# Kernel tuning notes

Hardware: AMD Instinct MI355X
Metric: run time of the kernel (lower is better)

Reference implementation:

```python
import jax, jax.numpy as jnp
import numpy as np

INPUT_DIM = 100
LATENT_DIM = 128
HIDDEN_DIM = 64
BATCH = 16384


def setup_inputs() -> dict:
    key = jax.random.key(0)
    ku, k1, kb1, k2, kb2 = jax.random.split(key, 5)
    u = jax.random.normal(ku, (BATCH, INPUT_DIM), dtype=jnp.float32)
    # PyTorch Linear init: U(-1/sqrt(fan_in), 1/sqrt(fan_in))
    s1 = 1.0 / np.sqrt(INPUT_DIM)
    s2 = 1.0 / np.sqrt(HIDDEN_DIM)
    W1 = jax.random.uniform(k1, (LATENT_DIM, HIDDEN_DIM, INPUT_DIM), jnp.float32, -s1, s1)
    b1 = jax.random.uniform(kb1, (LATENT_DIM, HIDDEN_DIM), jnp.float32, -s1, s1)
    W2 = jax.random.uniform(k2, (LATENT_DIM, HIDDEN_DIM), jnp.float32, -s2, s2)  # out_features=1 squeezed
    b2 = jax.random.uniform(kb2, (LATENT_DIM,), jnp.float32, -s2, s2)
    return {"u": u, "W1": W1, "b1": b1, "W2": W2, "b2": b2}


def reference(u, W1, b1, W2, b2):
    # All latent_dim branches batched as one grouped GEMM.
    # h: [batch, latent, hidden]
    h = jnp.tanh(jnp.einsum('bi,khi->bkh', u, W1) + b1[None, :, :])
    # out: [batch, latent]  (second Linear has output dim 1, squeezed)
    out = jnp.einsum('bkh,kh->bk', h, W2) + b2[None, :]
    return out
```

## Files before the change

### kernel.cpp

```cpp
#include <hip/hip_runtime.h>

#define BATCH 16384
#define LATENT 128
#define HIDDEN 64
#define INDIM 100
#define KPAD 128
#define TANH_SCALE 2.885390081777927f

typedef short shortx8 __attribute__((ext_vector_type(8)));
typedef float floatx4 __attribute__((ext_vector_type(4)));

__device__ __forceinline__ short f2bf(float f) {
    union { float f; unsigned u; } v; v.f = f;
    unsigned r = v.u + 0x7FFF + ((v.u >> 16) & 1);
    return (short)(r >> 16);
}

#if __has_builtin(__builtin_amdgcn_exp2f)
#define EXP2F(x) __builtin_amdgcn_exp2f(x)
#else
#define EXP2F(x) __exp2f(x)
#endif
#if __has_builtin(__builtin_amdgcn_rcpf)
#define RCPF(x) __builtin_amdgcn_rcpf(x)
#else
#define RCPF(x) (1.0f / (x))
#endif

#define N_U_CHUNKS (BATCH * KPAD / 8)
#define N_W_CHUNKS (LATENT * HIDDEN * KPAD / 8)

__global__ __launch_bounds__(256) void prep_all(const float* __restrict__ u,
                                                const float* __restrict__ W1,
                                                const float* __restrict__ b1,
                                                const float* __restrict__ W2,
                                                const float* __restrict__ b2,
                                                shortx8* __restrict__ uf,
                                                shortx8* __restrict__ wf,
                                                float* __restrict__ b2eff) {
    int c = blockIdx.x * 256 + threadIdx.x;
    if (c < N_U_CHUNKS) {
        int lane = c & 63;
        int kt = (c >> 6) & 3;
        int g = c >> 8;
        int row = g * 16 + (lane & 15);
        int kbase = kt * 32 + ((lane >> 4) << 3);
        shortx8 v;
        if (kbase + 7 < INDIM) {
            const float4* p = (const float4*)(u + row * INDIM + kbase);
            float4 f0 = p[0], f1 = p[1];
            v[0] = f2bf(f0.x); v[1] = f2bf(f0.y); v[2] = f2bf(f0.z); v[3] = f2bf(f0.w);
            v[4] = f2bf(f1.x); v[5] = f2bf(f1.y); v[6] = f2bf(f1.z); v[7] = f2bf(f1.w);
        } else {
#pragma unroll
            for (int j = 0; j < 8; j++) {
                int k = kbase + j;
                float f = (k < INDIM) ? u[row * INDIM + k] : (k == INDIM ? 1.0f : 0.0f);
                v[j] = f2bf(f);
            }
        }
        uf[c] = v;
    } else if (c < N_U_CHUNKS + N_W_CHUNKS) {
        int c2 = c - N_U_CHUNKS;
        int lane = c2 & 63;
        int kt = (c2 >> 6) & 3;
        int nt = (c2 >> 8) & 3;
        int lat = c2 >> 10;
        int h = nt * 16 + (lane & 15);
        int hw = lat * HIDDEN + h;
        int kbase = kt * 32 + ((lane >> 4) << 3);
        shortx8 v;
        if (kbase + 7 < INDIM) {
            const float4* p = (const float4*)(W1 + hw * INDIM + kbase);
            float4 f0 = p[0], f1 = p[1];
            v[0] = f2bf(f0.x * TANH_SCALE); v[1] = f2bf(f0.y * TANH_SCALE);
            v[2] = f2bf(f0.z * TANH_SCALE); v[3] = f2bf(f0.w * TANH_SCALE);
            v[4] = f2bf(f1.x * TANH_SCALE); v[5] = f2bf(f1.y * TANH_SCALE);
            v[6] = f2bf(f1.z * TANH_SCALE); v[7] = f2bf(f1.w * TANH_SCALE);
        } else {
#pragma unroll
            for (int j = 0; j < 8; j++) {
                int k = kbase + j;
                float f = (k < INDIM) ? W1[hw * INDIM + k] * TANH_SCALE
                                      : (k == INDIM ? b1[hw] * TANH_SCALE : 0.0f);
                v[j] = f2bf(f);
            }
        }
        wf[c2] = v;
    } else {
        int lat = c - (N_U_CHUNKS + N_W_CHUNKS);
        if (lat < LATENT) {
            float s = b2[lat];
            const float* wp = W2 + lat * HIDDEN;
#pragma unroll 8
            for (int h = 0; h < HIDDEN; h++) s += wp[h];
            b2eff[lat] = s;
        }
    }
}

__global__ __launch_bounds__(256, 4) void branch_mlp(const shortx8* __restrict__ uf,
                                                     const shortx8* __restrict__ wf,
                                                     const float* __restrict__ W2,
                                                     const float* __restrict__ b2eff,
                                                     float* __restrict__ out) {
    int tid = threadIdx.x;
    int lane = tid & 63;
    int w = tid >> 6;
    int bx = blockIdx.x;
    int lat = bx >> 5;
    int G0 = (bx & 31) * 32 + w * 8;
    int q = lane >> 4;

    shortx8 afr[4][4];
    const shortx8* wb = wf + (size_t)lat * 16 * 64 + lane;
#pragma unroll
    for (int nt = 0; nt < 4; nt++)
#pragma unroll
        for (int kt = 0; kt < 4; kt++)
            afr[nt][kt] = wb[(nt * 4 + kt) * 64];

    float4 w2v[4];
#pragma unroll
    for (int nt = 0; nt < 4; nt++) {
        float4 t = *(const float4*)(W2 + lat * HIDDEN + nt * 16 + q * 4);
        w2v[nt] = make_float4(-2.0f * t.x, -2.0f * t.y, -2.0f * t.z, -2.0f * t.w);
    }
    float b2v = b2eff[lat];

    const shortx8* ua = uf + (size_t)G0 * 4 * 64 + lane;
    float* outp = out + (size_t)G0 * 16 * LATENT + lat;

#pragma unroll
    for (int g = 0; g < 8; g++) {
        shortx8 ub[4];
#pragma unroll
        for (int kt = 0; kt < 4; kt++)
            ub[kt] = ua[(g * 4 + kt) * 64];

        floatx4 acc[4] = {};
#pragma unroll
        for (int kt = 0; kt < 4; kt++)
#pragma unroll
            for (int nt = 0; nt < 4; nt++)
                acc[nt] = __builtin_amdgcn_mfma_f32_16x16x32_bf16(afr[nt][kt], ub[kt], acc[nt], 0, 0, 0);

        float s = 0.0f;
#pragma unroll
        for (int nt = 0; nt < 4; nt++)
#pragma unroll
            for (int r = 0; r < 4; r++) {
                float e = EXP2F(acc[nt][r]);
                float rr = RCPF(e + 1.0f);
                s = fmaf((&w2v[nt].x)[r], rr, s);
            }
        s += __shfl_xor(s, 16, 64);
        s += __shfl_xor(s, 32, 64);
        if (lane < 16)
            outp[(g * 16 + lane) * LATENT] = s + b2v;
    }
}

__global__ __launch_bounds__(256) void fallback_kernel(const float* __restrict__ u, const float* __restrict__ W1,
                                                       const float* __restrict__ b1, const float* __restrict__ W2,
                                                       const float* __restrict__ b2, float* __restrict__ out) {
    int idx = blockIdx.x * 256 + threadIdx.x;
    if (idx >= BATCH * LATENT) return;
    int b = idx >> 7;
    int lat = idx & 127;
    const float* ub = u + b * INDIM;
    float s = 0.0f;
    for (int h = 0; h < HIDDEN; h++) {
        const float* wp = W1 + (lat * HIDDEN + h) * INDIM;
        float dd = b1[lat * HIDDEN + h];
        for (int k = 0; k < INDIM; k++) dd += ub[k] * wp[k];
        s += tanhf(dd) * W2[lat * HIDDEN + h];
    }
    out[idx] = s + b2[lat];
}

extern "C" void kernel_launch(void* const* d_in, const int* in_sizes, int n_in,
                              void* d_out, int out_size, void* d_ws, size_t ws_size,
                              hipStream_t stream) {
    const float* u  = (const float*)d_in[0];
    const float* W1 = (const float*)d_in[1];
    const float* b1 = (const float*)d_in[2];
    const float* W2 = (const float*)d_in[3];
    const float* b2 = (const float*)d_in[4];
    float* out = (float*)d_out;

    const size_t UF_BYTES = (size_t)BATCH * KPAD * 2;
    const size_t WF_BYTES = (size_t)LATENT * HIDDEN * KPAD * 2;
    const size_t B2_BYTES = LATENT * sizeof(float);

    if (ws_size < UF_BYTES + WF_BYTES + B2_BYTES) {
        fallback_kernel<<<(BATCH * LATENT + 255) / 256, 256, 0, stream>>>(u, W1, b1, W2, b2, out);
        return;
    }

    shortx8* uf = (shortx8*)d_ws;
    shortx8* wf = (shortx8*)((char*)d_ws + UF_BYTES);
    float* b2eff = (float*)((char*)d_ws + UF_BYTES + WF_BYTES);

    prep_all<<<(N_U_CHUNKS + N_W_CHUNKS) / 256 + 1, 256, 0, stream>>>(u, W1, b1, W2, b2, uf, wf, b2eff);
    branch_mlp<<<4096, 256, 0, stream>>>(uf, wf, W2, b2eff, out);
}
```

Baseline: 111.7 us.

## Split hidden dimension across waves and reduce partial sums in shared memory

```diff
diff --git a/kernel.cpp b/kernel.cpp
--- a/kernel.cpp
+++ b/kernel.cpp
@@ -99,7 +99,7 @@
     }
 }
 
-__global__ __launch_bounds__(256, 4) void branch_mlp(const shortx8* __restrict__ uf,
+__global__ __launch_bounds__(256, 6) void branch_mlp(const shortx8* __restrict__ uf,
                                                      const shortx8* __restrict__ wf,
                                                      const float* __restrict__ W2,
                                                      const float* __restrict__ b2eff,
@@ -108,28 +108,24 @@
     int lane = tid & 63;
     int w = tid >> 6;
     int bx = blockIdx.x;
-    int lat = bx >> 5;
-    int G0 = (bx & 31) * 32 + w * 8;
+    int lat = bx >> 7;
+    int G0 = (bx & 127) * 8;
     int q = lane >> 4;
 
-    shortx8 afr[4][4];
-    const shortx8* wb = wf + (size_t)lat * 16 * 64 + lane;
-#pragma unroll
-    for (int nt = 0; nt < 4; nt++)
-#pragma unroll
-        for (int kt = 0; kt < 4; kt++)
-            afr[nt][kt] = wb[(nt * 4 + kt) * 64];
-
-    float4 w2v[4];
-#pragma unroll
-    for (int nt = 0; nt < 4; nt++) {
-        float4 t = *(const float4*)(W2 + lat * HIDDEN + nt * 16 + q * 4);
-        w2v[nt] = make_float4(-2.0f * t.x, -2.0f * t.y, -2.0f * t.z, -2.0f * t.w);
-    }
+    __shared__ float red[4][128];
+
+    shortx8 afr[4];
+    const shortx8* wb = wf + (size_t)lat * 16 * 64 + (size_t)w * 4 * 64 + lane;
+#pragma unroll
+    for (int kt = 0; kt < 4; kt++)
+        afr[kt] = wb[kt * 64];
+
+    float4 t = *(const float4*)(W2 + lat * HIDDEN + w * 16 + q * 4);
+    float4 w2v = make_float4(-2.0f * t.x, -2.0f * t.y, -2.0f * t.z, -2.0f * t.w);
     float b2v = b2eff[lat];
 
     const shortx8* ua = uf + (size_t)G0 * 4 * 64 + lane;
-    float* outp = out + (size_t)G0 * 16 * LATENT + lat;
+    float s_arr[8];
 
 #pragma unroll
     for (int g = 0; g < 8; g++) {
@@ -138,26 +134,39 @@
         for (int kt = 0; kt < 4; kt++)
             ub[kt] = ua[(g * 4 + kt) * 64];
 
-        floatx4 acc[4] = {};
+        floatx4 acc = {};
 #pragma unroll
         for (int kt = 0; kt < 4; kt++)
-#pragma unroll
-            for (int nt = 0; nt < 4; nt++)
-                acc[nt] = __builtin_amdgcn_mfma_f32_16x16x32_bf16(afr[nt][kt], ub[kt], acc[nt], 0, 0, 0);
+            acc = __builtin_amdgcn_mfma_f32_16x16x32_bf16(afr[kt], ub[kt], acc, 0, 0, 0);
 
         float s = 0.0f;
 #pragma unroll
-        for (int nt = 0; nt < 4; nt++)
-#pragma unroll
-            for (int r = 0; r < 4; r++) {
-                float e = EXP2F(acc[nt][r]);
-                float rr = RCPF(e + 1.0f);
-                s = fmaf((&w2v[nt].x)[r], rr, s);
-            }
+        for (int r = 0; r < 4; r++) {
+            float e = EXP2F(acc[r]);
+            float rr = RCPF(e + 1.0f);
+            s = fmaf((&w2v.x)[r], rr, s);
+        }
         s += __shfl_xor(s, 16, 64);
         s += __shfl_xor(s, 32, 64);
-        if (lane < 16)
-            outp[(g * 16 + lane) * LATENT] = s + b2v;
+        s_arr[g] = s;
+    }
+
+    if (lane < 16) {
+#pragma unroll
+        for (int g = 0; g < 8; g++)
+            red[w][g * 16 + lane] = s_arr[g];
+    }
+    __syncthreads();
+
+    if (lane < 16) {
+        float* outp = out + (size_t)G0 * 16 * LATENT + lat;
+#pragma unroll
+        for (int j = 0; j < 2; j++) {
+            int g = w * 2 + j;
+            float s = red[0][g * 16 + lane] + red[1][g * 16 + lane] +
+                      red[2][g * 16 + lane] + red[3][g * 16 + lane] + b2v;
+            outp[(g * 16 + lane) * LATENT] = s;
+        }
     }
 }
 
@@ -203,5 +212,5 @@
     float* b2eff = (float*)((char*)d_ws + UF_BYTES + WF_BYTES);
 
     prep_all<<<(N_U_CHUNKS + N_W_CHUNKS) / 256 + 1, 256, 0, stream>>>(u, W1, b1, W2, b2, uf, wf, b2eff);
-    branch_mlp<<<4096, 256, 0, stream>>>(uf, wf, W2, b2eff, out);
-}
+    branch_mlp<<<16384, 256, 0, stream>>>(uf, wf, W2, b2eff, out);
+}
```

Result: slower. 147.9 us (+32.4%).
